# Optimization experiments

Measured on AMD Instinct MI355X. Metric: run time of the kernel, lower is better.

Reference implementation:

```python
import jax, jax.numpy as jnp
import numpy as np

FLOAT_MIN = jnp.finfo(jnp.float32).min


def setup_inputs() -> dict:
    key = jax.random.key(0)
    ks = jax.random.split(key, 8)
    B, S, F1, F2, A = 65536, 256, 256, 256, 128
    return {
        "obs_state": jax.random.normal(ks[0], (B, S), dtype=jnp.float32),
        "action_mask": jax.random.randint(ks[1], (B, A), 0, 2, dtype=jnp.int32),
        "W1": jax.random.normal(ks[2], (S, F1), dtype=jnp.float32) * (1.0 / np.sqrt(S)),
        "b1": jnp.zeros((F1,), dtype=jnp.float32),
        "W2": jax.random.normal(ks[3], (F1, F2), dtype=jnp.float32) * (1.0 / np.sqrt(F1)),
        "b2": jnp.zeros((F2,), dtype=jnp.float32),
        "W3": jax.random.normal(ks[4], (F2, A), dtype=jnp.float32) * (1.0 / np.sqrt(F2)),
        "b3": jnp.zeros((A,), dtype=jnp.float32),
    }


def reference(obs_state, action_mask, W1, b1, W2, b2, W3, b3):
    # 3-layer MLP: state -> fc1 -> relu -> fc2 -> relu -> fc3
    h = jax.nn.relu(obs_state @ W1 + b1)
    h = jax.nn.relu(h @ W2 + b2)
    x = h @ W3 + b3  # [B, A] logits

    # Vectorized action masking (replaces per-element Python loop):
    #   mask==0 -> FLOAT_MIN; rows with all-zero mask -> FLOAT_MIN everywhere, col 0 = 1.0
    valid = action_mask != 0  # [B, A] bool
    x = jnp.where(valid, x, FLOAT_MIN)
    all_invalid = ~jnp.any(valid, axis=1, keepdims=True)  # [B, 1]
    col0 = jnp.arange(x.shape[1]) == 0  # [A]
    x = jnp.where(all_invalid & col0, jnp.float32(1.0), x)
    return x
```

## Files before the change

kernel.cpp:

```cpp
#include <hip/hip_runtime.h>

typedef __attribute__((ext_vector_type(8))) short short8;
typedef __attribute__((ext_vector_type(8))) unsigned short ushort8;
typedef __attribute__((ext_vector_type(4))) float f32x4;

#define MT 32
#define STR 264

__device__ __forceinline__ float bmax_r18() { return __uint_as_float(0x7F7F0000u); }

__device__ __forceinline__ unsigned short f2bf_r18(float f) {
    unsigned int u = __float_as_uint(f);
    return (unsigned short)((u + 0x7fffu + ((u >> 16) & 1u)) >> 16);
}

__global__ __launch_bounds__(256)
void pack_weights_r18(const float* __restrict__ W1,
                      const float* __restrict__ W2,
                      const float* __restrict__ W3,
                      unsigned short* __restrict__ ws) {
    int s = blockIdx.x * 256 + threadIdx.x;
    const float* src;
    unsigned short* dst;
    int N;
    if (s < 8192)       { src = W1; dst = ws;          N = 256; }
    else if (s < 16384) { src = W2; dst = ws + 65536;  N = 256; s -= 8192; }
    else                { src = W3; dst = ws + 131072; N = 128; s -= 16384; }
    int frag = s >> 6, lane = s & 63;
    int kb = (frag & 7) * 32 + (lane >> 4) * 8;
    int n  = (frag >> 3) * 16 + (lane & 15);
    ushort8 o;
    #pragma unroll
    for (int j = 0; j < 8; ++j) o[j] = f2bf_r18(src[(kb + j) * N + n]);
    *(ushort8*)&dst[s * 8] = o;
}

__global__ __launch_bounds__(128, 4)
void ColorNetwork_32495722561720_kernel(
        const float* __restrict__ obs,
        const int* __restrict__ amask,
        const float* __restrict__ b1,
        const float* __restrict__ b2,
        const float* __restrict__ b3,
        const unsigned short* __restrict__ w1p,
        const unsigned short* __restrict__ w2p,
        const unsigned short* __restrict__ w3p,
        float* __restrict__ out)
{
    __shared__ __align__(16) unsigned short act[MT * STR];
    __shared__ int rowany[MT];

    const int tid  = threadIdx.x;
    const int wave = tid >> 6;
    const int lane = tid & 63;
    const int quad = lane >> 4;
    const int noff = lane & 15;
    const size_t rowbase = (size_t)blockIdx.x * MT;

    if (tid < MT) rowany[tid] = 0;

    {
        const float4* xin = (const float4*)(obs + rowbase * 256);
        #pragma unroll 4
        for (int i = 0; i < 16; ++i) {
            int f = tid + i * 128;
            int row = f >> 6;
            int c4 = f & 63;
            float4 v = xin[f];
            ushort4 p;
            p.x = f2bf_r18(v.x); p.y = f2bf_r18(v.y);
            p.z = f2bf_r18(v.z); p.w = f2bf_r18(v.w);
            *(ushort4*)&act[row * STR + c4 * 4] = p;
        }
    }
    __syncthreads();

    {
        const int4* min4 = (const int4*)(amask + rowbase * 128);
        #pragma unroll 4
        for (int i = 0; i < 8; ++i) {
            int f = tid + i * 128;
            int4 m = min4[f];
            if (m.x | m.y | m.z | m.w) rowany[f >> 5] = 1;
        }
    }

    short8 a[2][8];

    #pragma unroll
    for (int rt = 0; rt < 2; ++rt)
        #pragma unroll
        for (int k0 = 0; k0 < 8; ++k0)
            a[rt][k0] = *(const short8*)&act[(rt * 16 + noff) * STR + k0 * 32 + quad * 8];
    __syncthreads();
    #pragma unroll 2
    for (int ct = 0; ct < 8; ++ct) {
        const int ctg = wave * 8 + ct;
        f32x4 ac0 = {}, ac1 = {};
        #pragma unroll
        for (int k0 = 0; k0 < 8; ++k0) {
            short8 b = *(const short8*)&w1p[((ctg * 8 + k0) * 64 + lane) * 8];
            ac0 = __builtin_amdgcn_mfma_f32_16x16x32_bf16(a[0][k0], b, ac0, 0, 0, 0);
            ac1 = __builtin_amdgcn_mfma_f32_16x16x32_bf16(a[1][k0], b, ac1, 0, 0, 0);
        }
        const int col = ctg * 16 + noff;
        const float bv = b1[col];
        #pragma unroll
        for (int i = 0; i < 4; ++i) {
            act[(quad * 4 + i) * STR + col]      = f2bf_r18(fmaxf(ac0[i] + bv, 0.0f));
            act[(16 + quad * 4 + i) * STR + col] = f2bf_r18(fmaxf(ac1[i] + bv, 0.0f));
        }
    }
    __syncthreads();

    #pragma unroll
    for (int rt = 0; rt < 2; ++rt)
        #pragma unroll
        for (int k0 = 0; k0 < 8; ++k0)
            a[rt][k0] = *(const short8*)&act[(rt * 16 + noff) * STR + k0 * 32 + quad * 8];
    __syncthreads();
    #pragma unroll 2
    for (int ct = 0; ct < 8; ++ct) {
        const int ctg = wave * 8 + ct;
        f32x4 ac0 = {}, ac1 = {};
        #pragma unroll
        for (int k0 = 0; k0 < 8; ++k0) {
            short8 b = *(const short8*)&w2p[((ctg * 8 + k0) * 64 + lane) * 8];
            ac0 = __builtin_amdgcn_mfma_f32_16x16x32_bf16(a[0][k0], b, ac0, 0, 0, 0);
            ac1 = __builtin_amdgcn_mfma_f32_16x16x32_bf16(a[1][k0], b, ac1, 0, 0, 0);
        }
        const int col = ctg * 16 + noff;
        const float bv = b2[col];
        #pragma unroll
        for (int i = 0; i < 4; ++i) {
            act[(quad * 4 + i) * STR + col]      = f2bf_r18(fmaxf(ac0[i] + bv, 0.0f));
            act[(16 + quad * 4 + i) * STR + col] = f2bf_r18(fmaxf(ac1[i] + bv, 0.0f));
        }
    }
    __syncthreads();

    #pragma unroll
    for (int rt = 0; rt < 2; ++rt)
        #pragma unroll
        for (int k0 = 0; k0 < 8; ++k0)
            a[rt][k0] = *(const short8*)&act[(rt * 16 + noff) * STR + k0 * 32 + quad * 8];

    int ra[8];
    #pragma unroll
    for (int rt = 0; rt < 2; ++rt)
        #pragma unroll
        for (int i = 0; i < 4; ++i)
            ra[rt * 4 + i] = rowany[rt * 16 + quad * 4 + i];

    const float BM = bmax_r18();
    #pragma unroll 2
    for (int ct = 0; ct < 4; ++ct) {
        const int ctg = wave * 4 + ct;
        f32x4 ac0 = {}, ac1 = {};
        #pragma unroll
        for (int k0 = 0; k0 < 8; ++k0) {
            short8 b = *(const short8*)&w3p[((ctg * 8 + k0) * 64 + lane) * 8];
            ac0 = __builtin_amdgcn_mfma_f32_16x16x32_bf16(a[0][k0], b, ac0, 0, 0, 0);
            ac1 = __builtin_amdgcn_mfma_f32_16x16x32_bf16(a[1][k0], b, ac1, 0, 0, 0);
        }
        const int col = ctg * 16 + noff;
        const float bv = b3[col];
        #pragma unroll
        for (int rt = 0; rt < 2; ++rt) {
            const f32x4& ac = rt ? ac1 : ac0;
            #pragma unroll
            for (int i = 0; i < 4; ++i) {
                int row = rt * 16 + quad * 4 + i;
                int m = amask[(rowbase + row) * 128 + col];
                float v = ac[i] + bv;
                v = fminf(fmaxf(v, -BM), BM);
                if (!(v == v)) v = 0.0f;
                if (!m) v = -BM;
                if (!ra[rt * 4 + i]) v = (col == 0) ? 1.0f : -BM;
                out[(rowbase + row) * 128 + col] = v;
            }
        }
    }
}

extern "C" void kernel_launch(void* const* d_in, const int* in_sizes, int n_in,
                              void* d_out, int out_size, void* d_ws, size_t ws_size,
                              hipStream_t stream) {
    const float* obs   = (const float*)d_in[0];
    const int*   amask = (const int*)d_in[1];
    const float* W1 = (const float*)d_in[2];
    const float* b1 = (const float*)d_in[3];
    const float* W2 = (const float*)d_in[4];
    const float* b2 = (const float*)d_in[5];
    const float* W3 = (const float*)d_in[6];
    const float* b3 = (const float*)d_in[7];
    float* out = (float*)d_out;

    const int B = in_sizes[0] / 256;

    unsigned short* ws = (unsigned short*)d_ws;
    unsigned short* w1p = ws;
    unsigned short* w2p = ws + 65536;
    unsigned short* w3p = ws + 131072;

    pack_weights_r18<<<80, 256, 0, stream>>>(W1, W2, W3, ws);

    ColorNetwork_32495722561720_kernel<<<B / MT, 128, 0, stream>>>(
        obs, amask, b1, b2, b3, w1p, w2p, w3p, out);
}
```

Measured before the change: 165.8 us.

## Double-buffer weight fragment loads in registers across column tiles

Each layer now preloads the B-operand weight fragments for two column tiles into registers and prefetches the next tile's fragments while the current tile's MFMAs run. This hides global/L2 latency for the weight loads. The register demand this adds is handled by lowering launch_bounds occupancy from 4 to 3 blocks per CU. The input conversion loop unroll also goes from 4 to 8.

```diff
diff --git a/kernel.cpp b/kernel.cpp
--- a/kernel.cpp
+++ b/kernel.cpp
@@ -7,15 +7,15 @@
 #define MT 32
 #define STR 264
 
-__device__ __forceinline__ float bmax_r18() { return __uint_as_float(0x7F7F0000u); }
-
-__device__ __forceinline__ unsigned short f2bf_r18(float f) {
+__device__ __forceinline__ float bmax_r19() { return __uint_as_float(0x7F7F0000u); }
+
+__device__ __forceinline__ unsigned short f2bf_r19(float f) {
     unsigned int u = __float_as_uint(f);
     return (unsigned short)((u + 0x7fffu + ((u >> 16) & 1u)) >> 16);
 }
 
 __global__ __launch_bounds__(256)
-void pack_weights_r18(const float* __restrict__ W1,
+void pack_weights_r19(const float* __restrict__ W1,
                       const float* __restrict__ W2,
                       const float* __restrict__ W3,
                       unsigned short* __restrict__ ws) {
@@ -31,11 +31,69 @@
     int n  = (frag >> 3) * 16 + (lane & 15);
     ushort8 o;
     #pragma unroll
-    for (int j = 0; j < 8; ++j) o[j] = f2bf_r18(src[(kb + j) * N + n]);
+    for (int j = 0; j < 8; ++j) o[j] = f2bf_r19(src[(kb + j) * N + n]);
     *(ushort8*)&dst[s * 8] = o;
 }
 
-__global__ __launch_bounds__(128, 4)
+__device__ __forceinline__ void ldb8_r19(short8 b[8],
+                                         const unsigned short* __restrict__ wp,
+                                         int ctg, int lane) {
+    #pragma unroll
+    for (int k0 = 0; k0 < 8; ++k0)
+        b[k0] = *(const short8*)&wp[((ctg * 8 + k0) * 64 + lane) * 8];
+}
+
+__device__ __forceinline__ void ct_mfma_r19(const short8 a0[8], const short8 a1[8],
+                                            const short8 b[8], f32x4& ac0, f32x4& ac1) {
+    #pragma unroll
+    for (int k0 = 0; k0 < 8; ++k0) {
+        ac0 = __builtin_amdgcn_mfma_f32_16x16x32_bf16(a0[k0], b[k0], ac0, 0, 0, 0);
+        ac1 = __builtin_amdgcn_mfma_f32_16x16x32_bf16(a1[k0], b[k0], ac1, 0, 0, 0);
+    }
+}
+
+__device__ __forceinline__ void ct_store_r19(unsigned short* __restrict__ act,
+                                             const float* __restrict__ bias,
+                                             int ctg, int quad, int noff,
+                                             const f32x4& ac0, const f32x4& ac1) {
+    const int col = ctg * 16 + noff;
+    const float bv = bias[col];
+    #pragma unroll
+    for (int i = 0; i < 4; ++i) {
+        act[(quad * 4 + i) * STR + col]      = f2bf_r19(fmaxf(ac0[i] + bv, 0.0f));
+        act[(16 + quad * 4 + i) * STR + col] = f2bf_r19(fmaxf(ac1[i] + bv, 0.0f));
+    }
+}
+
+__device__ __forceinline__ void layer_r19(unsigned short* __restrict__ act,
+                                          const unsigned short* __restrict__ wp,
+                                          const float* __restrict__ bias,
+                                          int ctbase, int lane, int quad, int noff) {
+    short8 a0[8], a1[8];
+    #pragma unroll
+    for (int k0 = 0; k0 < 8; ++k0) {
+        a0[k0] = *(const short8*)&act[noff * STR + k0 * 32 + quad * 8];
+        a1[k0] = *(const short8*)&act[(16 + noff) * STR + k0 * 32 + quad * 8];
+    }
+    short8 bA[8], bB[8];
+    ldb8_r19(bA, wp, ctbase + 0, lane);
+    ldb8_r19(bB, wp, ctbase + 1, lane);
+    __syncthreads();
+    #pragma unroll 1
+    for (int pr = 0; pr < 4; ++pr) {
+        const int ct0 = ctbase + 2 * pr;
+        f32x4 e0 = {}, e1 = {};
+        ct_mfma_r19(a0, a1, bA, e0, e1);
+        if (pr < 3) ldb8_r19(bA, wp, ct0 + 2, lane);
+        ct_store_r19(act, bias, ct0, quad, noff, e0, e1);
+        f32x4 o0 = {}, o1 = {};
+        ct_mfma_r19(a0, a1, bB, o0, o1);
+        if (pr < 3) ldb8_r19(bB, wp, ct0 + 3, lane);
+        ct_store_r19(act, bias, ct0 + 1, quad, noff, o0, o1);
+    }
+}
+
+__global__ __launch_bounds__(128, 3)
 void ColorNetwork_32495722561720_kernel(
         const float* __restrict__ obs,
         const int* __restrict__ amask,
@@ -61,15 +119,15 @@
 
     {
         const float4* xin = (const float4*)(obs + rowbase * 256);
-        #pragma unroll 4
+        #pragma unroll 8
         for (int i = 0; i < 16; ++i) {
             int f = tid + i * 128;
             int row = f >> 6;
             int c4 = f & 63;
             float4 v = xin[f];
             ushort4 p;
-            p.x = f2bf_r18(v.x); p.y = f2bf_r18(v.y);
-            p.z = f2bf_r18(v.z); p.w = f2bf_r18(v.w);
+            p.x = f2bf_r19(v.x); p.y = f2bf_r19(v.y);
+            p.z = f2bf_r19(v.z); p.w = f2bf_r19(v.w);
             *(ushort4*)&act[row * STR + c4 * 4] = p;
         }
     }
@@ -85,99 +143,62 @@
         }
     }
 
-    short8 a[2][8];
-
-    #pragma unroll
-    for (int rt = 0; rt < 2; ++rt)
-        #pragma unroll
-        for (int k0 = 0; k0 < 8; ++k0)
-            a[rt][k0] = *(const short8*)&act[(rt * 16 + noff) * STR + k0 * 32 + quad * 8];
-    __syncthreads();
-    #pragma unroll 2
-    for (int ct = 0; ct < 8; ++ct) {
-        const int ctg = wave * 8 + ct;
-        f32x4 ac0 = {}, ac1 = {};
+    layer_r19(act, w1p, b1, wave * 8, lane, quad, noff);
+    __syncthreads();
+
+    layer_r19(act, w2p, b2, wave * 8, lane, quad, noff);
+    __syncthreads();
+
+    {
+        short8 a0[8], a1[8];
         #pragma unroll
         for (int k0 = 0; k0 < 8; ++k0) {
-            short8 b = *(const short8*)&w1p[((ctg * 8 + k0) * 64 + lane) * 8];
-            ac0 = __builtin_amdgcn_mfma_f32_16x16x32_bf16(a[0][k0], b, ac0, 0, 0, 0);
-            ac1 = __builtin_amdgcn_mfma_f32_16x16x32_bf16(a[1][k0], b, ac1, 0, 0, 0);
-        }
-        const int col = ctg * 16 + noff;
-        const float bv = b1[col];
+            a0[k0] = *(const short8*)&act[noff * STR + k0 * 32 + quad * 8];
+            a1[k0] = *(const short8*)&act[(16 + noff) * STR + k0 * 32 + quad * 8];
+        }
+        const int ctbase = wave * 4;
+        short8 bA[8], bB[8];
+        ldb8_r19(bA, w3p, ctbase + 0, lane);
+        ldb8_r19(bB, w3p, ctbase + 1, lane);
+
+        int ra[8];
         #pragma unroll
-        for (int i = 0; i < 4; ++i) {
-            act[(quad * 4 + i) * STR + col]      = f2bf_r18(fmaxf(ac0[i] + bv, 0.0f));
-            act[(16 + quad * 4 + i) * STR + col] = f2bf_r18(fmaxf(ac1[i] + bv, 0.0f));
-        }
-    }
-    __syncthreads();
-
-    #pragma unroll
-    for (int rt = 0; rt < 2; ++rt)
-        #pragma unroll
-        for (int k0 = 0; k0 < 8; ++k0)
-            a[rt][k0] = *(const short8*)&act[(rt * 16 + noff) * STR + k0 * 32 + quad * 8];
-    __syncthreads();
-    #pragma unroll 2
-    for (int ct = 0; ct < 8; ++ct) {
-        const int ctg = wave * 8 + ct;
-        f32x4 ac0 = {}, ac1 = {};
-        #pragma unroll
-        for (int k0 = 0; k0 < 8; ++k0) {
-            short8 b = *(const short8*)&w2p[((ctg * 8 + k0) * 64 + lane) * 8];
-            ac0 = __builtin_amdgcn_mfma_f32_16x16x32_bf16(a[0][k0], b, ac0, 0, 0, 0);
-            ac1 = __builtin_amdgcn_mfma_f32_16x16x32_bf16(a[1][k0], b, ac1, 0, 0, 0);
-        }
-        const int col = ctg * 16 + noff;
-        const float bv = b2[col];
-        #pragma unroll
-        for (int i = 0; i < 4; ++i) {
-            act[(quad * 4 + i) * STR + col]      = f2bf_r18(fmaxf(ac0[i] + bv, 0.0f));
-            act[(16 + quad * 4 + i) * STR + col] = f2bf_r18(fmaxf(ac1[i] + bv, 0.0f));
-        }
-    }
-    __syncthreads();
-
-    #pragma unroll
-    for (int rt = 0; rt < 2; ++rt)
-        #pragma unroll
-        for (int k0 = 0; k0 < 8; ++k0)
-            a[rt][k0] = *(const short8*)&act[(rt * 16 + noff) * STR + k0 * 32 + quad * 8];
-
-    int ra[8];
-    #pragma unroll
-    for (int rt = 0; rt < 2; ++rt)
-        #pragma unroll
-        for (int i = 0; i < 4; ++i)
-            ra[rt * 4 + i] = rowany[rt * 16 + quad * 4 + i];
-
-    const float BM = bmax_r18();
-    #pragma unroll 2
-    for (int ct = 0; ct < 4; ++ct) {
-        const int ctg = wave * 4 + ct;
-        f32x4 ac0 = {}, ac1 = {};
-        #pragma unroll
-        for (int k0 = 0; k0 < 8; ++k0) {
-            short8 b = *(const short8*)&w3p[((ctg * 8 + k0) * 64 + lane) * 8];
-            ac0 = __builtin_amdgcn_mfma_f32_16x16x32_bf16(a[0][k0], b, ac0, 0, 0, 0);
-            ac1 = __builtin_amdgcn_mfma_f32_16x16x32_bf16(a[1][k0], b, ac1, 0, 0, 0);
-        }
-        const int col = ctg * 16 + noff;
-        const float bv = b3[col];
-        #pragma unroll
-        for (int rt = 0; rt < 2; ++rt) {
-            const f32x4& ac = rt ? ac1 : ac0;
+        for (int rt = 0; rt < 2; ++rt)
             #pragma unroll
-            for (int i = 0; i < 4; ++i) {
-                int row = rt * 16 + quad * 4 + i;
-                int m = amask[(rowbase + row) * 128 + col];
-                float v = ac[i] + bv;
-                v = fminf(fmaxf(v, -BM), BM);
-                if (!(v == v)) v = 0.0f;
-                if (!m) v = -BM;
-                if (!ra[rt * 4 + i]) v = (col == 0) ? 1.0f : -BM;
-                out[(rowbase + row) * 128 + col] = v;
+            for (int i = 0; i < 4; ++i)
+                ra[rt * 4 + i] = rowany[rt * 16 + quad * 4 + i];
+
+        const float BM = bmax_r19();
+        #pragma unroll 1
+        for (int pr = 0; pr < 2; ++pr) {
+            #pragma unroll
+            for (int half = 0; half < 2; ++half) {
+                const int ct = ctbase + 2 * pr + half;
+                f32x4 ac0 = {}, ac1 = {};
+                if (half == 0) {
+                    ct_mfma_r19(a0, a1, bA, ac0, ac1);
+                    if (pr < 1) ldb8_r19(bA, w3p, ct + 2, lane);
+                } else {
+                    ct_mfma_r19(a0, a1, bB, ac0, ac1);
+                    if (pr < 1) ldb8_r19(bB, w3p, ct + 2, lane);
+                }
+                const int col = ct * 16 + noff;
+                const float bv = b3[col];
+                #pragma unroll
+                for (int rt = 0; rt < 2; ++rt) {
+                    const f32x4& ac = rt ? ac1 : ac0;
+                    #pragma unroll
+                    for (int i = 0; i < 4; ++i) {
+                        int row = rt * 16 + quad * 4 + i;
+                        int m = amask[(rowbase + row) * 128 + col];
+                        float v = ac[i] + bv;
+                        v = fminf(fmaxf(v, -BM), BM);
+                        if (!(v == v)) v = 0.0f;
+                        if (!m) v = -BM;
+                        if (!ra[rt * 4 + i]) v = (col == 0) ? 1.0f : -BM;
+                        out[(rowbase + row) * 128 + col] = v;
+                    }
+                }
             }
         }
     }
@@ -203,7 +224,7 @@
     unsigned short* w2p = ws + 65536;
     unsigned short* w3p = ws + 131072;
 
-    pack_weights_r18<<<80, 256, 0, stream>>>(W1, W2, W3, ws);
+    pack_weights_r19<<<80, 256, 0, stream>>>(W1, W2, W3, ws);
 
     ColorNetwork_32495722561720_kernel<<<B / MT, 128, 0, stream>>>(
         obs, amask, b1, b2, b3, w1p, w2p, w3p, out);
```

Result: slower. 192.9 us (+16.3%).
